# Kernel tuning notes

Hardware: AMD Instinct MI355X
Metric: run time of the kernel (lower is better)

The kernel has to match this reference:

```python
import jax, jax.numpy as jnp
import numpy as np

K_HOPS = 10
ALPHA = 0.1
N_NODES = 50000
N_EDGES = 600000
F_IN = 128
HIDDEN = 64
N_CLASSES = 40


def setup_inputs() -> dict:
    key = jax.random.key(0)
    k1, k2, k3, k4 = jax.random.split(key, 4)
    x = jax.random.normal(k1, (N_NODES, F_IN), dtype=jnp.float32)
    edge_index = jax.random.randint(k2, (2, N_EDGES), 0, N_NODES, dtype=jnp.int32)
    edge_weight = jnp.ones((N_EDGES,), dtype=jnp.float32)
    W1 = jax.random.normal(k3, (F_IN, HIDDEN), dtype=jnp.float32) * (1.0 / np.sqrt(F_IN))
    b1 = jnp.zeros((HIDDEN,), dtype=jnp.float32)
    W2 = jax.random.normal(k4, (HIDDEN, N_CLASSES), dtype=jnp.float32) * (1.0 / np.sqrt(HIDDEN))
    b2 = jnp.zeros((N_CLASSES,), dtype=jnp.float32)
    return {"x": x, "edge_index": edge_index, "edge_weight": edge_weight,
            "W1": W1, "b1": b1, "W2": W2, "b2": b2}


def reference(x, edge_index, edge_weight, W1, b1, W2, b2):
    n = x.shape[0]
    # GCN symmetric normalization with self-loops (tfg gcn cache)
    self_idx = jnp.arange(n, dtype=edge_index.dtype)
    row = jnp.concatenate([edge_index[0], self_idx])
    col = jnp.concatenate([edge_index[1], self_idx])
    w = jnp.concatenate([edge_weight, jnp.ones((n,), dtype=edge_weight.dtype)])
    deg = jax.ops.segment_sum(w, row, num_segments=n)
    dinv = jnp.where(deg > 0, jax.lax.rsqrt(jnp.maximum(deg, 1e-12)), 0.0)
    nw = dinv[row] * w * dinv[col]  # [E+N] normalized edge weights

    def prop(h):
        # h_out[i] = sum_{(i,j)} nw * h[j]
        return jax.ops.segment_sum(h[col] * nw[:, None], row, num_segments=n)

    def step(h, _):
        h_next = prop(h)
        return h_next, None

    # SSGC: out = (1-alpha)/K * sum_{l=1..K} T^l x + alpha * x
    def step_acc(carry, _):
        h, acc = carry
        h_next = prop(h)
        return (h_next, acc + h_next), None

    (_, acc), _ = jax.lax.scan(step_acc, (x, jnp.zeros_like(x)), None, length=K_HOPS)
    h = (1.0 - ALPHA) / K_HOPS * acc + ALPHA * x  # [N, F]

    h = jax.nn.relu(h @ W1 + b1)  # [N, HIDDEN]
    logits = h @ W2 + b2          # [N, N_CLASSES]
    return logits
```

## Files before the change

### kernel.cpp

```cpp
#include <hip/hip_runtime.h>
#include <hip/hip_fp16.h>
#include <math.h>

constexpr int   N   = 50000;
constexpr int   E   = 600000;
constexpr int   FIN = 128;
constexpr int   H   = 64;
constexpr int   C   = 40;
constexpr int   K   = 10;
constexpr float CK  = (1.0f - 0.1f) / 10.0f;
constexpr float AL  = 0.1f;

constexpr int NBIN = (N + 63) / 64;
constexpr int HB   = (E + 1023) / 1024;
constexpr int M    = NBIN * HB;
constexpr int SB   = (M + 1023) / 1024;

typedef float v2f __attribute__((ext_vector_type(2)));

__device__ __forceinline__ unsigned pack_fp8x4(float f0, float f1, float f2, float f3) {
    unsigned r = __builtin_amdgcn_cvt_pk_fp8_f32(f0, f1, 0u, false);
    r = __builtin_amdgcn_cvt_pk_fp8_f32(f2, f3, r, true);
    return r;
}

__device__ __forceinline__ float ep_w(unsigned v) {
    return __half2float(__ushort_as_half((unsigned short)(v >> 16)));
}
__device__ __forceinline__ unsigned ep_pack(int c, float w) {
    return (unsigned)(unsigned short)c |
           ((unsigned)__half_as_ushort(__float2half_rn(w)) << 16);
}

__device__ __forceinline__ void accum4(float* s, unsigned v, float w) {
    v2f p0 = __builtin_amdgcn_cvt_pk_f32_fp8(v, false);
    v2f p1 = __builtin_amdgcn_cvt_pk_f32_fp8(v, true);
    s[0] = fmaf(w, p0.x, s[0]); s[1] = fmaf(w, p0.y, s[1]);
    s[2] = fmaf(w, p1.x, s[2]); s[3] = fmaf(w, p1.y, s[3]);
}

constexpr int G1N  = 64;
constexpr int XPAD = 132;
__global__ __launch_bounds__(256, 2) void k_gemm1(const float* __restrict__ x,
                                                  const float* __restrict__ W1,
                                                  float* __restrict__ y0,
                                                  unsigned char* __restrict__ y0f8) {
    __shared__ float ws[FIN * H];
    __shared__ float xs[G1N * XPAD];
    const float4* W14 = (const float4*)W1;
    const float4* x4  = (const float4*)x;
    int t = threadIdx.x;
    int node0 = blockIdx.x * G1N;
    for (int i = t; i < FIN * H / 4; i += 256) ((float4*)ws)[i] = W14[i];
    for (int p = 0; p < 8; ++p) {
        int idx = p * 256 + t;
        int n   = idx >> 5;
        int kk  = idx & 31;
        int node = node0 + n;
        float4 v = (node < N) ? x4[(size_t)node * (FIN / 4) + kk]
                              : make_float4(0.f, 0.f, 0.f, 0.f);
        *(float4*)(xs + n * XPAD + kk * 4) = v;
    }
    __syncthreads();
    int nb = (t >> 4) * 4;
    int cb = (t & 15) * 4;
    float a00=0,a01=0,a02=0,a03=0, a10=0,a11=0,a12=0,a13=0;
    float a20=0,a21=0,a22=0,a23=0, a30=0,a31=0,a32=0,a33=0;
#pragma unroll 8
    for (int k = 0; k < FIN; ++k) {
        float4 wv = *(const float4*)(ws + k * H + cb);
        float x0 = xs[(nb + 0) * XPAD + k];
        float x1 = xs[(nb + 1) * XPAD + k];
        float x2 = xs[(nb + 2) * XPAD + k];
        float x3 = xs[(nb + 3) * XPAD + k];
        a00 = fmaf(x0, wv.x, a00); a01 = fmaf(x0, wv.y, a01);
        a02 = fmaf(x0, wv.z, a02); a03 = fmaf(x0, wv.w, a03);
        a10 = fmaf(x1, wv.x, a10); a11 = fmaf(x1, wv.y, a11);
        a12 = fmaf(x1, wv.z, a12); a13 = fmaf(x1, wv.w, a13);
        a20 = fmaf(x2, wv.x, a20); a21 = fmaf(x2, wv.y, a21);
        a22 = fmaf(x2, wv.z, a22); a23 = fmaf(x2, wv.w, a23);
        a30 = fmaf(x3, wv.x, a30); a31 = fmaf(x3, wv.y, a31);
        a32 = fmaf(x3, wv.z, a32); a33 = fmaf(x3, wv.w, a33);
    }
    float4 rows[4] = {make_float4(a00,a01,a02,a03), make_float4(a10,a11,a12,a13),
                      make_float4(a20,a21,a22,a23), make_float4(a30,a31,a32,a33)};
#pragma unroll
    for (int i = 0; i < 4; ++i) {
        int node = node0 + nb + i;
        if (node >= N) break;
        float4 r = rows[i];
        *(float4*)(y0 + (size_t)node * H + cb) = r;
        *(unsigned*)(y0f8 + (size_t)node * H + cb) = pack_fp8x4(r.x, r.y, r.z, r.w);
    }
}

__global__ __launch_bounds__(256) void k_hist(const int* __restrict__ row,
                                              unsigned* __restrict__ bhT) {
    __shared__ unsigned h[NBIN];
    for (int i = threadIdx.x; i < NBIN; i += 256) h[i] = 0;
    __syncthreads();
    int b = blockIdx.x;
    int base = b * 1024 + threadIdx.x;
#pragma unroll
    for (int i = 0; i < 4; ++i) {
        int e = base + i * 256;
        if (e < E) atomicAdd(&h[row[e] >> 6], 1u);
    }
    __syncthreads();
    for (int i = threadIdx.x; i < NBIN; i += 256)
        bhT[(size_t)i * HB + b] = h[i];
}

__global__ __launch_bounds__(1024) void k_scan1(unsigned* __restrict__ S,
                                                unsigned* __restrict__ bsumA) {
    __shared__ unsigned s[1024];
    int gid = blockIdx.x * 1024 + threadIdx.x;
    unsigned v = (gid < M) ? S[gid] : 0;
    s[threadIdx.x] = v;
    __syncthreads();
    for (int off = 1; off < 1024; off <<= 1) {
        unsigned t = (threadIdx.x >= off) ? s[threadIdx.x - off] : 0;
        __syncthreads();
        s[threadIdx.x] += t;
        __syncthreads();
    }
    if (gid < M) S[gid] = s[threadIdx.x] - v;
    if (threadIdx.x == 1023) bsumA[blockIdx.x] = s[1023];
}

__global__ __launch_bounds__(512) void k_scan2(unsigned* __restrict__ bsumA) {
    __shared__ unsigned s[512];
    int t = threadIdx.x;
    unsigned v = (t < SB) ? bsumA[t] : 0;
    s[t] = v;
    __syncthreads();
    for (int off = 1; off < 512; off <<= 1) {
        unsigned x = (t >= off) ? s[t - off] : 0;
        __syncthreads();
        s[t] += x;
        __syncthreads();
    }
    if (t < SB) bsumA[t] = s[t] - v;
}

__global__ __launch_bounds__(256) void k_bucket(const int* __restrict__ row,
                                                const int* __restrict__ col,
                                                const float* __restrict__ w,
                                                const unsigned* __restrict__ S,
                                                const unsigned* __restrict__ bofs,
                                                unsigned long long* __restrict__ barr) {
    __shared__ unsigned cur[NBIN];
    int b = blockIdx.x;
    for (int i = threadIdx.x; i < NBIN; i += 256) {
        unsigned idx = (unsigned)i * HB + (unsigned)b;
        cur[i] = S[idx] + bofs[idx >> 10];
    }
    __syncthreads();
    int base = b * 1024 + threadIdx.x;
#pragma unroll
    for (int i = 0; i < 4; ++i) {
        int e = base + i * 256;
        if (e < E) {
            int r = row[e];
            unsigned p = atomicAdd(&cur[r >> 6], 1u);
            unsigned short wh = __half_as_ushort(__float2half_rn(w[e]));
            barr[p] = ((unsigned long long)wh << 32) |
                      ((unsigned long long)(unsigned)r << 16) |
                      (unsigned long long)(unsigned)col[e];
        }
    }
}

__device__ __forceinline__ unsigned bucket_lo(const unsigned* S, const unsigned* bofs,
                                              int bin) {
    unsigned idx = (unsigned)bin * HB;
    return S[idx] + bofs[idx >> 10];
}

__global__ __launch_bounds__(256) void k_cnt(const unsigned long long* __restrict__ barr,
                                             const unsigned* __restrict__ S,
                                             const unsigned* __restrict__ bofs,
                                             int* __restrict__ cnt) {
    __shared__ unsigned rc[64];
    if (threadIdx.x < 64) rc[threadIdx.x] = 0;
    __syncthreads();
    int bin = blockIdx.x;
    unsigned i0 = bucket_lo(S, bofs, bin);
    unsigned i1 = (bin + 1 < NBIN) ? bucket_lo(S, bofs, bin + 1) : (unsigned)E;
    for (unsigned i = i0 + threadIdx.x; i < i1; i += 256) {
        unsigned r = (unsigned)(barr[i] >> 16) & 0xFFFFu;
        atomicAdd(&rc[r & 63], 1u);
    }
    __syncthreads();
    int r0 = bin * 64;
    if (threadIdx.x < 64 && r0 + (int)threadIdx.x < N)
        cnt[r0 + threadIdx.x] = (int)rc[threadIdx.x];
}

__global__ __launch_bounds__(1024) void k_scan_blocks(const int* __restrict__ cnt,
                                                      int* __restrict__ row_ptr,
                                                      int* __restrict__ bsum) {
    __shared__ int s[1024];
    int gid = blockIdx.x * 1024 + threadIdx.x;
    int v = 0;
    if (gid < N) v = (cnt[gid] + 3) & ~3;
    s[threadIdx.x] = v;
    __syncthreads();
    for (int off = 1; off < 1024; off <<= 1) {
        int t = (threadIdx.x >= off) ? s[threadIdx.x - off] : 0;
        __syncthreads();
        s[threadIdx.x] += t;
        __syncthreads();
    }
    if (gid < N) row_ptr[gid] = s[threadIdx.x] - v;
    if (threadIdx.x == 1023) bsum[blockIdx.x] = s[1023];
}

constexpr int NB = (N + 1023) / 1024;
__global__ __launch_bounds__(1024) void k_addoff(int* __restrict__ row_ptr,
                                                 const int* __restrict__ bsum,
                                                 const int* __restrict__ cnt,
                                                 unsigned* __restrict__ ep) {
    __shared__ int sboff;
    __shared__ int stot;
    if (threadIdx.x < 64) {
        int lane = threadIdx.x;
        int orig = (lane < NB) ? bsum[lane] : 0;
        int v = orig;
        for (int off = 1; off < 64; off <<= 1) {
            int t = __shfl_up(v, off, 64);
            if (lane >= off) v += t;
        }
        if (lane == (int)blockIdx.x) sboff = v - orig;
        if (lane == NB - 1)          stot  = v;
    }
    __syncthreads();
    int gid = blockIdx.x * 1024 + threadIdx.x;
    if (gid < N) {
        int rp = row_ptr[gid] + sboff;
        row_ptr[gid] = rp;
        int real = cnt[gid];
        int pd = (real + 3) & ~3;
        for (int j = real; j < pd; ++j) ep[rp + j] = 0u;
    }
    if (gid == 0) {
        row_ptr[N] = stot;
        *(uint4*)(ep + stot) = make_uint4(0u, 0u, 0u, 0u);
    }
}

__global__ __launch_bounds__(256) void k_emit(const unsigned long long* __restrict__ barr,
                                              const unsigned* __restrict__ S,
                                              const unsigned* __restrict__ bofs,
                                              const int* __restrict__ row_ptr,
                                              unsigned* __restrict__ ep) {
    __shared__ unsigned cur[64];
    int bin = blockIdx.x;
    int r0 = bin * 64;
    if (threadIdx.x < 64) {
        int r = r0 + (int)threadIdx.x;
        cur[threadIdx.x] = (r < N) ? (unsigned)row_ptr[r] : 0u;
    }
    __syncthreads();
    unsigned i0 = bucket_lo(S, bofs, bin);
    unsigned i1 = (bin + 1 < NBIN) ? bucket_lo(S, bofs, bin + 1) : (unsigned)E;
    for (unsigned i = i0 + threadIdx.x; i < i1; i += 256) {
        unsigned long long v = barr[i];
        unsigned r = (unsigned)(v >> 16) & 0xFFFFu;
        unsigned p = atomicAdd(&cur[r & 63], 1u);
        ep[p] = (unsigned)(v & 0xFFFFu) | (((unsigned)(v >> 32) & 0xFFFFu) << 16);
    }
}

__global__ __launch_bounds__(256) void k_deg_dinv(const unsigned* __restrict__ ep,
                                                  const int* __restrict__ row_ptr,
                                                  float* __restrict__ dinv,
                                                  float* __restrict__ dinv2) {
    int node = blockIdx.x * 32 + (threadIdx.x >> 3);
    if (node >= N) return;
    int l = threadIdx.x & 7;
    int e0 = row_ptr[node], e1 = row_ptr[node + 1];
    float d = 0.f;
    for (int j4 = (e0 >> 2) + l; j4 * 4 < e1; j4 += 8) {
        uint4 v = ((const uint4*)ep)[j4];
        d += ep_w(v.x) + ep_w(v.y) + ep_w(v.z) + ep_w(v.w);
    }
    d += __shfl_xor(d, 1, 64);
    d += __shfl_xor(d, 2, 64);
    d += __shfl_xor(d, 4, 64);
    if (l == 0) {
        d += 1.0f;
        float di = rsqrtf(d);
        dinv[node]  = di;
        dinv2[node] = di * di;
    }
}

__global__ __launch_bounds__(256) void k_norm(unsigned* __restrict__ ep,
                                              const int* __restrict__ row_ptr,
                                              const float* __restrict__ dinv) {
    int node = blockIdx.x * 32 + (threadIdx.x >> 3);
    if (node >= N) return;
    int l = threadIdx.x & 7;
    float dr = dinv[node];
    int e0 = row_ptr[node], e1 = row_ptr[node + 1];
    for (int j4 = (e0 >> 2) + l; j4 * 4 < e1; j4 += 8) {
        uint4 v = ((uint4*)ep)[j4];
        v.x = ep_pack(v.x & 0xFFFFu, ep_w(v.x) * dr * dinv[v.x & 0xFFFFu]);
        v.y = ep_pack(v.y & 0xFFFFu, ep_w(v.y) * dr * dinv[v.y & 0xFFFFu]);
        v.z = ep_pack(v.z & 0xFFFFu, ep_w(v.z) * dr * dinv[v.z & 0xFFFFu]);
        v.w = ep_pack(v.w & 0xFFFFu, ep_w(v.w) * dr * dinv[v.w & 0xFFFFu]);
        ((uint4*)ep)[j4] = v;
    }
}

constexpr int HSP = 68;
template <bool WRITE_H, bool ACC_INIT, bool FINAL>
__global__ __launch_bounds__(256) void k_prop(const unsigned* __restrict__ hin,
                                              unsigned* __restrict__ hout,
                                              __half* __restrict__ acch,
                                              const float* __restrict__ dinv2,
                                              const int* __restrict__ row_ptr,
                                              const unsigned* __restrict__ ep,
                                              const float4* __restrict__ y04,
                                              const float* __restrict__ b1,
                                              const float* __restrict__ W2,
                                              const float* __restrict__ b2,
                                              float* __restrict__ out) {
    extern __shared__ float smem[];
    float* w2s = smem;
    float* hs  = smem + H * C;
    float* b2s = hs + 16 * HSP;
    float* b1s = b2s + C;
    int t = threadIdx.x;
    if (FINAL) {
        for (int i = t; i < H * C; i += 256) w2s[i] = W2[i];
        if (t < C) b2s[t] = b2[t];
        if (t < H) b1s[t] = b1[t];
        __syncthreads();
    }
    int lane = t & 63;
    int nib  = (t >> 6) * 4 + (lane >> 4);
    int l    = lane & 15;
    int node = blockIdx.x * 16 + nib;
    bool nv  = node < N;
    int nodec = nv ? node : N - 1;
    int start = row_ptr[nodec];
    int pdeg  = nv ? (row_ptr[nodec + 1] - start) : 0;
    int md = pdeg;
#pragma unroll
    for (int off = 16; off <= 32; off <<= 1) md = max(md, __shfl_xor(md, off, 64));

    size_t base = (size_t)nodec * 16 + l;
    unsigned vself = hin[base];
    float d2       = dinv2[nodec];
    uint2* ap = (uint2*)(acch + (size_t)nodec * H + l * 4);
    uint2 old;
    if (nv && (FINAL || !ACC_INIT)) old = *ap;

    float s[4];
#pragma unroll
    for (int i = 0; i < 4; ++i) s[i] = 0.f;

    const unsigned* rp = ep + start;
    uint4 ea = *(const uint4*)rp;
    uint4 eb = *(const uint4*)(rp + ((4 < pdeg) ? 4 : 0));
    for (int batch = 0; batch < md; batch += 8) {
        uint4 ca = ea, cb = eb;
        int n0 = batch + 8, n1 = batch + 12;
        ea = *(const uint4*)(rp + ((n0 < pdeg) ? n0 : 0));
        eb = *(const uint4*)(rp + ((n1 < pdeg) ? n1 : 0));
        unsigned v0 = hin[(size_t)(ca.x & 0xFFFFu) * 16 + l];
        unsigned v1 = hin[(size_t)(ca.y & 0xFFFFu) * 16 + l];
        unsigned v2 = hin[(size_t)(ca.z & 0xFFFFu) * 16 + l];
        unsigned v3 = hin[(size_t)(ca.w & 0xFFFFu) * 16 + l];
        unsigned v4 = hin[(size_t)(cb.x & 0xFFFFu) * 16 + l];
        unsigned v5 = hin[(size_t)(cb.y & 0xFFFFu) * 16 + l];
        unsigned v6 = hin[(size_t)(cb.z & 0xFFFFu) * 16 + l];
        unsigned v7 = hin[(size_t)(cb.w & 0xFFFFu) * 16 + l];
        accum4(s, v0, (batch     < pdeg) ? ep_w(ca.x) : 0.0f);
        accum4(s, v1, (batch + 1 < pdeg) ? ep_w(ca.y) : 0.0f);
        accum4(s, v2, (batch + 2 < pdeg) ? ep_w(ca.z) : 0.0f);
        accum4(s, v3, (batch + 3 < pdeg) ? ep_w(ca.w) : 0.0f);
        accum4(s, v4, (batch + 4 < pdeg) ? ep_w(cb.x) : 0.0f);
        accum4(s, v5, (batch + 5 < pdeg) ? ep_w(cb.y) : 0.0f);
        accum4(s, v6, (batch + 6 < pdeg) ? ep_w(cb.z) : 0.0f);
        accum4(s, v7, (batch + 7 < pdeg) ? ep_w(cb.w) : 0.0f);
    }
    if (nv) {
        accum4(s, vself, d2);
        if (WRITE_H) {
            hout[base] = pack_fp8x4(s[0], s[1], s[2], s[3]);
        }
        if (FINAL) {
            const unsigned* u = (const unsigned*)&old;
#pragma unroll
            for (int d = 0; d < 2; ++d) {
                float2 f = __half22float2(*(__half2*)&u[d]);
                s[2*d+0] += f.x; s[2*d+1] += f.y;
            }
            float4 ya = y04[(size_t)nodec * (H / 4) + l];
            const float* bp = b1s + l * 4;
            float* hp = hs + nib * HSP + l * 4;
            hp[0] = fmaxf(fmaf(CK, s[0], fmaf(AL, ya.x, bp[0])), 0.f);
            hp[1] = fmaxf(fmaf(CK, s[1], fmaf(AL, ya.y, bp[1])), 0.f);
            hp[2] = fmaxf(fmaf(CK, s[2], fmaf(AL, ya.z, bp[2])), 0.f);
            hp[3] = fmaxf(fmaf(CK, s[3], fmaf(AL, ya.w, bp[3])), 0.f);
        } else {
            if (!ACC_INIT) {
                const unsigned* u = (const unsigned*)&old;
#pragma unroll
                for (int d = 0; d < 2; ++d) {
                    float2 f = __half22float2(*(__half2*)&u[d]);
                    s[2*d+0] += f.x; s[2*d+1] += f.y;
                }
            }
            uint2 nvp;
            unsigned* u = (unsigned*)&nvp;
#pragma unroll
            for (int d = 0; d < 2; ++d) {
                __half2 h = __floats2half2_rn(s[2*d+0], s[2*d+1]);
                u[d] = *(unsigned*)&h;
            }
            *ap = nvp;
        }
    }
    if (FINAL) {
        __syncthreads();
        int node0 = blockIdx.x * 16;
        for (int o = t; o < 16 * C; o += 256) {
            int nl = o / C, c = o % C;
            int n2 = node0 + nl;
            if (n2 >= N) continue;
            float v = b2s[c];
            const float* hr = &hs[nl * HSP];
#pragma unroll
            for (int k = 0; k < H; ++k) v = fmaf(hr[k], w2s[k * C + c], v);
            out[n2 * C + c] = v;
        }
    }
}

extern "C" void kernel_launch(void* const* d_in, const int* in_sizes, int n_in,
                              void* d_out, int out_size, void* d_ws, size_t ws_size,
                              hipStream_t stream) {
    const float* x  = (const float*)d_in[0];
    const int*   ei = (const int*)d_in[1];
    const float* ew = (const float*)d_in[2];
    const float* W1 = (const float*)d_in[3];
    const float* b1 = (const float*)d_in[4];
    const float* W2 = (const float*)d_in[5];
    const float* b2 = (const float*)d_in[6];
    float* out = (float*)d_out;

    const int* row = ei;
    const int* col = ei + E;

    char* ws = (char*)d_ws;
    size_t off = 0;
    auto alloc = [&](size_t bytes) -> char* {
        char* p = ws + off;
        off = (off + bytes + 1023) & ~(size_t)1023;
        return p;
    };
    constexpr size_t EPAD = (size_t)E + 3 * (size_t)N + 1024;
    float*              y0    = (float*)alloc((size_t)N * H * 4);
    unsigned char*      y0f8  = (unsigned char*)alloc((size_t)N * H);
    unsigned char*      ha    = (unsigned char*)alloc((size_t)N * H);
    unsigned char*      hb    = (unsigned char*)alloc((size_t)N * H);
    __half*             acch  = (__half*)alloc((size_t)N * H * 2);
    int*                cnt   = (int*)alloc((size_t)N * 4);
    unsigned*           bhT   = (unsigned*)alloc((size_t)M * 4);
    unsigned*           bsumA = (unsigned*)alloc(512 * 4);
    unsigned long long* barr  = (unsigned long long*)alloc((size_t)E * 8);
    float*    dinv    = (float*)alloc((size_t)N * 4);
    float*    dinv2   = (float*)alloc((size_t)N * 4);
    int*      row_ptr = (int*)alloc((size_t)(N + 1) * 4);
    int*      bsum    = (int*)alloc(64 * 4);
    unsigned* ep      = (unsigned*)alloc(EPAD * 4);

    k_gemm1<<<(N + G1N - 1) / G1N, 256, 0, stream>>>(x, W1, y0, y0f8);

    k_hist  <<<HB, 256, 0, stream>>>(row, bhT);
    k_scan1 <<<SB, 1024, 0, stream>>>(bhT, bsumA);
    k_scan2 <<<1, 512, 0, stream>>>(bsumA);
    k_bucket<<<HB, 256, 0, stream>>>(row, col, ew, bhT, bsumA, barr);
    k_cnt   <<<NBIN, 256, 0, stream>>>(barr, bhT, bsumA, cnt);

    k_scan_blocks<<<NB, 1024, 0, stream>>>(cnt, row_ptr, bsum);
    k_addoff<<<NB, 1024, 0, stream>>>(row_ptr, bsum, cnt, ep);

    k_emit<<<NBIN, 256, 0, stream>>>(barr, bhT, bsumA, row_ptr, ep);
    k_deg_dinv<<<(N + 31) / 32, 256, 0, stream>>>(ep, row_ptr, dinv, dinv2);
    k_norm<<<(N + 31) / 32, 256, 0, stream>>>(ep, row_ptr, dinv);

    const unsigned* hin = (const unsigned*)y0f8;
    unsigned* bufs[2] = {(unsigned*)ha, (unsigned*)hb};
    const float4* y04 = (const float4*)y0;
    int grid = (N + 15) / 16;
    size_t smemF = (size_t)(H * C + 16 * HSP + C + H) * 4;
    for (int hop = 0; hop < K; ++hop) {
        unsigned* hout = bufs[hop & 1];
        if (hop == 0)
            k_prop<true, true, false><<<grid, 256, 0, stream>>>(hin, hout, acch, dinv2,
                row_ptr, ep, y04, b1, W2, b2, out);
        else if (hop == K - 1)
            k_prop<false, false, true><<<grid, 256, smemF, stream>>>(hin, hout, acch, dinv2,
                row_ptr, ep, y04, b1, W2, b2, out);
        else
            k_prop<true, false, false><<<grid, 256, 0, stream>>>(hin, hout, acch, dinv2,
                row_ptr, ep, y04, b1, W2, b2, out);
        hin = hout;
    }
}
```

Measured before the change: 279.9 us.

## Fuse degree computation into emit and store per-hop results separately for a final MLP

The degree/dinv computation moves into k_emit, using shared-memory float atomics per bin, which removes one pass over the edge array and one kernel launch. Each propagation hop now writes its own fp16 result slice with nontemporal stores instead of read-modify-writing a running accumulator. A separate k_mlp kernel then sums the ten slices and runs the dense head. This drops the per-hop accumulator read and the template branching, at the cost of ten times the accumulator workspace and an extra kernel that rereads all slices.

Result: no change. 277.9 us (-0.7%).

```diff
diff --git a/kernel.cpp b/kernel.cpp
--- a/kernel.cpp
+++ b/kernel.cpp
@@ -253,13 +253,17 @@
                                               const unsigned* __restrict__ S,
                                               const unsigned* __restrict__ bofs,
                                               const int* __restrict__ row_ptr,
-                                              unsigned* __restrict__ ep) {
+                                              unsigned* __restrict__ ep,
+                                              float* __restrict__ dinv,
+                                              float* __restrict__ dinv2) {
     __shared__ unsigned cur[64];
+    __shared__ float wsum[64];
     int bin = blockIdx.x;
     int r0 = bin * 64;
     if (threadIdx.x < 64) {
         int r = r0 + (int)threadIdx.x;
         cur[threadIdx.x] = (r < N) ? (unsigned)row_ptr[r] : 0u;
+        wsum[threadIdx.x] = 0.f;
     }
     __syncthreads();
     unsigned i0 = bucket_lo(S, bofs, bin);
@@ -267,32 +271,20 @@
     for (unsigned i = i0 + threadIdx.x; i < i1; i += 256) {
         unsigned long long v = barr[i];
         unsigned r = (unsigned)(v >> 16) & 0xFFFFu;
+        unsigned wh = (unsigned)(v >> 32) & 0xFFFFu;
         unsigned p = atomicAdd(&cur[r & 63], 1u);
-        ep[p] = (unsigned)(v & 0xFFFFu) | (((unsigned)(v >> 32) & 0xFFFFu) << 16);
-    }
-}
-
-__global__ __launch_bounds__(256) void k_deg_dinv(const unsigned* __restrict__ ep,
-                                                  const int* __restrict__ row_ptr,
-                                                  float* __restrict__ dinv,
-                                                  float* __restrict__ dinv2) {
-    int node = blockIdx.x * 32 + (threadIdx.x >> 3);
-    if (node >= N) return;
-    int l = threadIdx.x & 7;
-    int e0 = row_ptr[node], e1 = row_ptr[node + 1];
-    float d = 0.f;
-    for (int j4 = (e0 >> 2) + l; j4 * 4 < e1; j4 += 8) {
-        uint4 v = ((const uint4*)ep)[j4];
-        d += ep_w(v.x) + ep_w(v.y) + ep_w(v.z) + ep_w(v.w);
-    }
-    d += __shfl_xor(d, 1, 64);
-    d += __shfl_xor(d, 2, 64);
-    d += __shfl_xor(d, 4, 64);
-    if (l == 0) {
-        d += 1.0f;
-        float di = rsqrtf(d);
-        dinv[node]  = di;
-        dinv2[node] = di * di;
+        ep[p] = (unsigned)(v & 0xFFFFu) | (wh << 16);
+        atomicAdd(&wsum[r & 63], __half2float(__ushort_as_half((unsigned short)wh)));
+    }
+    __syncthreads();
+    if (threadIdx.x < 64) {
+        int r = r0 + (int)threadIdx.x;
+        if (r < N) {
+            float d = 1.0f + wsum[threadIdx.x];
+            float di = rsqrtf(d);
+            dinv[r]  = di;
+            dinv2[r] = di * di;
+        }
     }
 }
 
@@ -314,31 +306,14 @@
     }
 }
 
-constexpr int HSP = 68;
-template <bool WRITE_H, bool ACC_INIT, bool FINAL>
+template <bool WRITE_H>
 __global__ __launch_bounds__(256) void k_prop(const unsigned* __restrict__ hin,
                                               unsigned* __restrict__ hout,
-                                              __half* __restrict__ acch,
+                                              __half* __restrict__ haccl,
                                               const float* __restrict__ dinv2,
                                               const int* __restrict__ row_ptr,
-                                              const unsigned* __restrict__ ep,
-                                              const float4* __restrict__ y04,
-                                              const float* __restrict__ b1,
-                                              const float* __restrict__ W2,
-                                              const float* __restrict__ b2,
-                                              float* __restrict__ out) {
-    extern __shared__ float smem[];
-    float* w2s = smem;
-    float* hs  = smem + H * C;
-    float* b2s = hs + 16 * HSP;
-    float* b1s = b2s + C;
+                                              const unsigned* __restrict__ ep) {
     int t = threadIdx.x;
-    if (FINAL) {
-        for (int i = t; i < H * C; i += 256) w2s[i] = W2[i];
-        if (t < C) b2s[t] = b2[t];
-        if (t < H) b1s[t] = b1[t];
-        __syncthreads();
-    }
     int lane = t & 63;
     int nib  = (t >> 6) * 4 + (lane >> 4);
     int l    = lane & 15;
@@ -354,9 +329,6 @@
     size_t base = (size_t)nodec * 16 + l;
     unsigned vself = hin[base];
     float d2       = dinv2[nodec];
-    uint2* ap = (uint2*)(acch + (size_t)nodec * H + l * 4);
-    uint2 old;
-    if (nv && (FINAL || !ACC_INIT)) old = *ap;
 
     float s[4];
 #pragma unroll
@@ -392,52 +364,64 @@
         if (WRITE_H) {
             hout[base] = pack_fp8x4(s[0], s[1], s[2], s[3]);
         }
-        if (FINAL) {
-            const unsigned* u = (const unsigned*)&old;
-#pragma unroll
-            for (int d = 0; d < 2; ++d) {
-                float2 f = __half22float2(*(__half2*)&u[d]);
-                s[2*d+0] += f.x; s[2*d+1] += f.y;
-            }
-            float4 ya = y04[(size_t)nodec * (H / 4) + l];
-            const float* bp = b1s + l * 4;
-            float* hp = hs + nib * HSP + l * 4;
-            hp[0] = fmaxf(fmaf(CK, s[0], fmaf(AL, ya.x, bp[0])), 0.f);
-            hp[1] = fmaxf(fmaf(CK, s[1], fmaf(AL, ya.y, bp[1])), 0.f);
-            hp[2] = fmaxf(fmaf(CK, s[2], fmaf(AL, ya.z, bp[2])), 0.f);
-            hp[3] = fmaxf(fmaf(CK, s[3], fmaf(AL, ya.w, bp[3])), 0.f);
-        } else {
-            if (!ACC_INIT) {
-                const unsigned* u = (const unsigned*)&old;
-#pragma unroll
-                for (int d = 0; d < 2; ++d) {
-                    float2 f = __half22float2(*(__half2*)&u[d]);
-                    s[2*d+0] += f.x; s[2*d+1] += f.y;
-                }
-            }
-            uint2 nvp;
-            unsigned* u = (unsigned*)&nvp;
-#pragma unroll
-            for (int d = 0; d < 2; ++d) {
-                __half2 h = __floats2half2_rn(s[2*d+0], s[2*d+1]);
-                u[d] = *(unsigned*)&h;
-            }
-            *ap = nvp;
+        __half2 h0 = __floats2half2_rn(s[0], s[1]);
+        __half2 h1 = __floats2half2_rn(s[2], s[3]);
+        unsigned long long acc64 =
+            ((unsigned long long)(*(unsigned*)&h1) << 32) | (*(unsigned*)&h0);
+        __builtin_nontemporal_store(acc64,
+            (unsigned long long*)(haccl + (size_t)nodec * H + l * 4));
+    }
+}
+
+constexpr int HSP = 68;
+__global__ __launch_bounds__(256) void k_mlp(const __half* __restrict__ hacc,
+                                             const float4* __restrict__ y04,
+                                             const float* __restrict__ b1,
+                                             const float* __restrict__ W2,
+                                             const float* __restrict__ b2,
+                                             float* __restrict__ out) {
+    __shared__ float w2s[H * C];
+    __shared__ float hs[16 * HSP];
+    __shared__ float b2s[C];
+    __shared__ float b1s[H];
+    int t = threadIdx.x;
+    for (int i = t; i < H * C; i += 256) w2s[i] = W2[i];
+    if (t < C) b2s[t] = b2[t];
+    if (t < H) b1s[t] = b1[t];
+    __syncthreads();
+    int lane = t & 63;
+    int nib  = (t >> 6) * 4 + (lane >> 4);
+    int l    = lane & 15;
+    int node = blockIdx.x * 16 + nib;
+    if (node < N) {
+        size_t off = (size_t)node * H + l * 4;
+        float s[4] = {0.f, 0.f, 0.f, 0.f};
+#pragma unroll
+        for (int k = 0; k < K; ++k) {
+            uint2 v = *(const uint2*)(hacc + (size_t)k * N * H + off);
+            float2 f0 = __half22float2(*(__half2*)&v.x);
+            float2 f1 = __half22float2(*(__half2*)&v.y);
+            s[0] += f0.x; s[1] += f0.y; s[2] += f1.x; s[3] += f1.y;
         }
-    }
-    if (FINAL) {
-        __syncthreads();
-        int node0 = blockIdx.x * 16;
-        for (int o = t; o < 16 * C; o += 256) {
-            int nl = o / C, c = o % C;
-            int n2 = node0 + nl;
-            if (n2 >= N) continue;
-            float v = b2s[c];
-            const float* hr = &hs[nl * HSP];
-#pragma unroll
-            for (int k = 0; k < H; ++k) v = fmaf(hr[k], w2s[k * C + c], v);
-            out[n2 * C + c] = v;
-        }
+        float4 ya = y04[(size_t)node * (H / 4) + l];
+        const float* bp = b1s + l * 4;
+        float* hp = hs + nib * HSP + l * 4;
+        hp[0] = fmaxf(fmaf(CK, s[0], fmaf(AL, ya.x, bp[0])), 0.f);
+        hp[1] = fmaxf(fmaf(CK, s[1], fmaf(AL, ya.y, bp[1])), 0.f);
+        hp[2] = fmaxf(fmaf(CK, s[2], fmaf(AL, ya.z, bp[2])), 0.f);
+        hp[3] = fmaxf(fmaf(CK, s[3], fmaf(AL, ya.w, bp[3])), 0.f);
+    }
+    __syncthreads();
+    int node0 = blockIdx.x * 16;
+    for (int o = t; o < 16 * C; o += 256) {
+        int nl = o / C, c = o % C;
+        int n2 = node0 + nl;
+        if (n2 >= N) continue;
+        float v = b2s[c];
+        const float* hr = &hs[nl * HSP];
+#pragma unroll
+        for (int k = 0; k < H; ++k) v = fmaf(hr[k], w2s[k * C + c], v);
+        out[n2 * C + c] = v;
     }
 }
 
@@ -468,7 +452,7 @@
     unsigned char*      y0f8  = (unsigned char*)alloc((size_t)N * H);
     unsigned char*      ha    = (unsigned char*)alloc((size_t)N * H);
     unsigned char*      hb    = (unsigned char*)alloc((size_t)N * H);
-    __half*             acch  = (__half*)alloc((size_t)N * H * 2);
+    __half*             hacc  = (__half*)alloc((size_t)K * N * H * 2);
     int*                cnt   = (int*)alloc((size_t)N * 4);
     unsigned*           bhT   = (unsigned*)alloc((size_t)M * 4);
     unsigned*           bsumA = (unsigned*)alloc(512 * 4);
@@ -490,26 +474,21 @@
     k_scan_blocks<<<NB, 1024, 0, stream>>>(cnt, row_ptr, bsum);
     k_addoff<<<NB, 1024, 0, stream>>>(row_ptr, bsum, cnt, ep);
 
-    k_emit<<<NBIN, 256, 0, stream>>>(barr, bhT, bsumA, row_ptr, ep);
-    k_deg_dinv<<<(N + 31) / 32, 256, 0, stream>>>(ep, row_ptr, dinv, dinv2);
+    k_emit<<<NBIN, 256, 0, stream>>>(barr, bhT, bsumA, row_ptr, ep, dinv, dinv2);
     k_norm<<<(N + 31) / 32, 256, 0, stream>>>(ep, row_ptr, dinv);
 
     const unsigned* hin = (const unsigned*)y0f8;
     unsigned* bufs[2] = {(unsigned*)ha, (unsigned*)hb};
     const float4* y04 = (const float4*)y0;
     int grid = (N + 15) / 16;
-    size_t smemF = (size_t)(H * C + 16 * HSP + C + H) * 4;
     for (int hop = 0; hop < K; ++hop) {
         unsigned* hout = bufs[hop & 1];
-        if (hop == 0)
-            k_prop<true, true, false><<<grid, 256, 0, stream>>>(hin, hout, acch, dinv2,
-                row_ptr, ep, y04, b1, W2, b2, out);
-        else if (hop == K - 1)
-            k_prop<false, false, true><<<grid, 256, smemF, stream>>>(hin, hout, acch, dinv2,
-                row_ptr, ep, y04, b1, W2, b2, out);
+        __half* haccl = hacc + (size_t)hop * N * H;
+        if (hop < K - 1)
+            k_prop<true><<<grid, 256, 0, stream>>>(hin, hout, haccl, dinv2, row_ptr, ep);
         else
-            k_prop<true, false, false><<<grid, 256, 0, stream>>>(hin, hout, acch, dinv2,
-                row_ptr, ep, y04, b1, W2, b2, out);
+            k_prop<false><<<grid, 256, 0, stream>>>(hin, hout, haccl, dinv2, row_ptr, ep);
         hin = hout;
     }
-}
+    k_mlp<<<grid, 256, 0, stream>>>(hacc, y04, b1, W2, b2, out);
+}
```
